# Kernel tuning notes

Measured on AMD Instinct MI355X. Metric: run time of the kernel, lower is better.

## Reference

```python
import jax, jax.numpy as jnp
import numpy as np

# FP4 (E2M1) code table: nibble = [sign(1) | exp(2) | mantissa(1)]
# magnitudes for codes 0..7: 0, 0.5, 1, 1.5, 2, 3, 4, 6; codes 8..15 are negated.
_MAG = np.array([0.0, 0.5, 1.0, 1.5, 2.0, 3.0, 4.0, 6.0], dtype=np.float32)
FP4_LUT = jnp.asarray(np.concatenate([_MAG, -_MAG]))  # [16]

BLOCK = 16  # scale-factor block size along in_features


def setup_inputs() -> dict:
    key = jax.random.key(0)
    k0, k1, k2, k3, k4 = jax.random.split(key, 5)
    M, K, N = 32, 8192, 8192  # tokens, in_features, out_features
    inp = jax.random.normal(k0, (M, K), dtype=jnp.float32)
    qweight = jax.random.randint(k1, (N, K // 2), 0, 256, dtype=jnp.int32)  # packed FP4 pairs
    scales = jax.random.uniform(k2, (N, K // BLOCK), dtype=jnp.float32)      # per-block scales
    amax = jax.random.uniform(k3, (1,), dtype=jnp.float32) + 0.5             # global scale
    bias = jax.random.normal(k4, (N,), dtype=jnp.float32)
    return {"input": inp, "qweight": qweight, "scales": scales, "amax": amax, "bias": bias}


def _dequantize(qweight, scales, amax):
    N = qweight.shape[0]
    low = qweight & 0xF            # first element of each pair
    high = (qweight >> 4) & 0xF    # second element
    nibbles = jnp.stack([low, high], axis=-1).reshape(N, -1)  # [N, K]
    vals = FP4_LUT[nibbles]                                   # [N, K] fp4 values
    # per-block scaling: block of BLOCK contiguous in-features shares one scale
    w = (vals.reshape(N, -1, BLOCK) * scales[..., None]).reshape(N, -1)
    return w * amax[0]


def reference(input, qweight, scales, amax, bias):
    weight = _dequantize(qweight, scales, amax)   # [N, K] full-precision weight
    return input @ weight.T + bias                # F.linear
```

## Files before the change

### kernel.cpp

```cpp
#include <hip/hip_runtime.h>
#include <hip/hip_bf16.h>

#define M_DIM 32
#define K_DIM 8192
#define N_DIM 8192
#define KS 16
#define KCH (K_DIM / KS)
#define STEPS (KCH / 32)
#define NPB 128
#define NBLK (N_DIM / NPB)
#define MAIN_BLOCKS (NBLK * KS)

#define QW_ROWI4 (K_DIM / 8)
#define SC_ROW (K_DIM / 16)

#define QROW 65
#define AROW 520
#define SROW 34

typedef _Float16 half8   __attribute__((ext_vector_type(8)));
typedef _Float16 half4_t __attribute__((ext_vector_type(4)));
typedef float    floatx4 __attribute__((ext_vector_type(4)));

__device__ __forceinline__ uint32_t dec2(uint32_t b) {
  uint32_t c0 = b & 0xFu, c1 = (b >> 4) & 0xFu;
  uint32_t m0 = c0 & 7u, m1 = c1 & 7u;
  uint32_t t0 = min(28u * m0, m0 + 28u);
  uint32_t t1 = min(28u * m1, m1 + 28u);
  return (t0 << 9) | ((c0 & 8u) << 12)
       | (t1 << 25) | ((c1 & 8u) << 28);
}

__device__ __forceinline__ half8 decode8p(uint32_t q, _Float16 s) {
  union { uint32_t u[4]; half8 h; } w;
  w.u[0] = dec2(q & 0xFFu);
  w.u[1] = dec2((q >> 8) & 0xFFu);
  w.u[2] = dec2((q >> 16) & 0xFFu);
  w.u[3] = dec2((q >> 24) & 0xFFu);
  half8 sv = {s, s, s, s, s, s, s, s};
  return w.h * sv;
}

__global__ void init_out_kernel(floatx4* __restrict__ out4,
                                const floatx4* __restrict__ bias4) {
  int idx = blockIdx.x * blockDim.x + threadIdx.x;
  out4[idx] = bias4[idx & (N_DIM / 4 - 1)];
}

__global__ void reduce_kernel(const floatx4* __restrict__ part,
                              const floatx4* __restrict__ bias4,
                              floatx4* __restrict__ out4) {
  int idx = blockIdx.x * blockDim.x + threadIdx.x;
  floatx4 acc = bias4[idx & (N_DIM / 4 - 1)];
#pragma unroll
  for (int s = 0; s < KS; ++s)
    acc += part[(size_t)s * (M_DIM * N_DIM / 4) + idx];
  out4[idx] = acc;
}

template <bool PARTIAL>
__global__ __launch_bounds__(256, 2) void fp4_linear_kernel(
    const float* __restrict__ inp,
    const int4*  __restrict__ qw4,
    const float* __restrict__ scales,
    const float* __restrict__ amaxp,
    float* __restrict__ outp)
{
  __shared__ uint32_t Qs[NPB * QROW];
  __shared__ _Float16 As[M_DIM * AROW];
  __shared__ _Float16 Ss[NPB * SROW];

  const int t    = threadIdx.x;
  const int lane = t & 63;
  const int w    = t >> 6;
  const int ks   = blockIdx.x & (KS - 1);
  const int nb   = blockIdx.x >> 4;
  const int n0   = nb * NPB;
  const float amax = amaxp[0];

  {
    const int4* qbase = qw4 + (size_t)ks * (KCH / 8);
    for (int g = 0; g < 4; ++g) {
      int4 tmp[8];
#pragma unroll
      for (int j = 0; j < 8; ++j) {
        const int r = w * 32 + g * 8 + j;
        tmp[j] = qbase[(size_t)(n0 + r) * QW_ROWI4 + lane];
      }
#pragma unroll
      for (int j = 0; j < 8; ++j) {
        const int r = w * 32 + g * 8 + j;
        uint32_t pk = ((uint32_t)tmp[j].x & 0xFFu)
                    | (((uint32_t)tmp[j].y & 0xFFu) << 8)
                    | (((uint32_t)tmp[j].z & 0xFFu) << 16)
                    | (((uint32_t)tmp[j].w & 0xFFu) << 24);
        Qs[r * QROW + lane] = pk;
      }
    }
  }

  {
    for (int g = 0; g < 2; ++g) {
      floatx4 tmp[8];
#pragma unroll
      for (int j = 0; j < 4; ++j) {
        const int r = w * 8 + g * 4 + j;
        const floatx4* ab =
            reinterpret_cast<const floatx4*>(inp + (size_t)r * K_DIM + ks * KCH);
        tmp[2 * j]     = ab[lane];
        tmp[2 * j + 1] = ab[lane + 64];
      }
#pragma unroll
      for (int j = 0; j < 4; ++j) {
        const int r = w * 8 + g * 4 + j;
        floatx4 f0 = tmp[2 * j], f1 = tmp[2 * j + 1];
        half4_t h0, h1;
        h0[0] = (_Float16)f0[0]; h0[1] = (_Float16)f0[1];
        h0[2] = (_Float16)f0[2]; h0[3] = (_Float16)f0[3];
        h1[0] = (_Float16)f1[0]; h1[1] = (_Float16)f1[1];
        h1[2] = (_Float16)f1[2]; h1[3] = (_Float16)f1[3];
        *(half4_t*)&As[r * AROW + lane * 4]        = h0;
        *(half4_t*)&As[r * AROW + (lane + 64) * 4] = h1;
      }
    }
  }

  {
#pragma unroll
    for (int j = 0; j < 4; ++j) {
      const int idx = j * 256 + t;
      const int r = idx >> 3, c = idx & 7;
      floatx4 f = reinterpret_cast<const floatx4*>(
          scales + (size_t)(n0 + r) * SC_ROW + ks * (KCH / 16))[c];
      half4_t h;
      h[0] = (_Float16)(f[0] * amax); h[1] = (_Float16)(f[1] * amax);
      h[2] = (_Float16)(f[2] * amax); h[3] = (_Float16)(f[3] * amax);
      *(half4_t*)&Ss[r * SROW + c * 4] = h;
    }
  }
  __syncthreads();

  const int row  = lane & 15;
  const int quad = lane >> 4;
  const int nloc = w * 32;

  const uint32_t* qAp = &Qs[(nloc + row) * QROW];
  const uint32_t* qBp = &Qs[(nloc + 16 + row) * QROW];
  const _Float16* a0p = &As[row * AROW];
  const _Float16* a1p = &As[(row + 16) * AROW];
  const _Float16* sAp = &Ss[(nloc + row) * SROW];
  const _Float16* sBp = &Ss[(nloc + 16 + row) * SROW];

  floatx4 acc00 = {0.f, 0.f, 0.f, 0.f};
  floatx4 acc01 = {0.f, 0.f, 0.f, 0.f};
  floatx4 acc10 = {0.f, 0.f, 0.f, 0.f};
  floatx4 acc11 = {0.f, 0.f, 0.f, 0.f};

#pragma unroll
  for (int it = 0; it < STEPS; ++it) {
    const uint32_t qA = qAp[it * 4 + quad];
    const uint32_t qB = qBp[it * 4 + quad];
    const _Float16 sA = sAp[it * 2 + (quad >> 1)];
    const _Float16 sB = sBp[it * 2 + (quad >> 1)];
    half8 bA = decode8p(qA, sA);
    half8 bB = decode8p(qB, sB);
    half8 a0 = *(const half8*)(a0p + it * 32 + quad * 8);
    half8 a1 = *(const half8*)(a1p + it * 32 + quad * 8);
    acc00 = __builtin_amdgcn_mfma_f32_16x16x32_f16(a0, bA, acc00, 0, 0, 0);
    acc01 = __builtin_amdgcn_mfma_f32_16x16x32_f16(a0, bB, acc01, 0, 0, 0);
    acc10 = __builtin_amdgcn_mfma_f32_16x16x32_f16(a1, bA, acc10, 0, 0, 0);
    acc11 = __builtin_amdgcn_mfma_f32_16x16x32_f16(a1, bB, acc11, 0, 0, 0);
  }

  if (PARTIAL) {
    float* pb = outp + (size_t)ks * (M_DIM * N_DIM);
#pragma unroll
    for (int r = 0; r < 4; ++r) {
      const int m = quad * 4 + r;
      float* o0 = pb + (size_t)m * N_DIM + n0 + nloc;
      float* o1 = pb + (size_t)(m + 16) * N_DIM + n0 + nloc;
      o0[row]      = acc00[r];
      o0[16 + row] = acc01[r];
      o1[row]      = acc10[r];
      o1[16 + row] = acc11[r];
    }
  } else {
#pragma unroll
    for (int r = 0; r < 4; ++r) {
      const int m = quad * 4 + r;
      float* o0 = outp + (size_t)m * N_DIM + n0 + nloc;
      float* o1 = outp + (size_t)(m + 16) * N_DIM + n0 + nloc;
      unsafeAtomicAdd(o0 + row,      acc00[r]);
      unsafeAtomicAdd(o0 + 16 + row, acc01[r]);
      unsafeAtomicAdd(o1 + row,      acc10[r]);
      unsafeAtomicAdd(o1 + 16 + row, acc11[r]);
    }
  }
}

extern "C" void kernel_launch(void* const* d_in, const int* in_sizes, int n_in,
                              void* d_out, int out_size, void* d_ws, size_t ws_size,
                              hipStream_t stream) {
  const float* inp    = (const float*)d_in[0];
  const int4*  qw4    = (const int4*)d_in[1];
  const float* scales = (const float*)d_in[2];
  const float* amaxp  = (const float*)d_in[3];
  const float* bias   = (const float*)d_in[4];
  float* out = (float*)d_out;

  const size_t part_bytes = (size_t)KS * M_DIM * N_DIM * sizeof(float);
  if (ws_size >= part_bytes) {
    float* part = (float*)d_ws;
    fp4_linear_kernel<true><<<MAIN_BLOCKS, 256, 0, stream>>>(
        inp, qw4, scales, amaxp, part);
    reduce_kernel<<<M_DIM * N_DIM / 4 / 256, 256, 0, stream>>>(
        (const floatx4*)part, (const floatx4*)bias, (floatx4*)out);
  } else {
    init_out_kernel<<<M_DIM * N_DIM / 4 / 256, 256, 0, stream>>>(
        (floatx4*)out, (const floatx4*)bias);
    fp4_linear_kernel<false><<<MAIN_BLOCKS, 256, 0, stream>>>(
        inp, qw4, scales, amaxp, out);
  }
}
```

Before: 224.4 us.

## Restructure split-K decomposition with fp16 activation pre-pass and in-block wave reduction

Changes the split-K layout from 16 K-slices with 128 output columns per block to 2 K-halves with 16 columns per block. Each wave now handles a quarter of the block's K range and the four waves are reduced through shared memory. A separate kernel converts the activations to fp16 once, and the main kernel then reads them straight from global memory instead of staging them per block. XOR swizzling is added to the weight and scale shared arrays. This shrinks the partial-sum buffer and the final reduction and raises occupancy. The costs are an extra launch, reliance on the workspace being large enough with the fallback path removed, and reading A from global memory without shared-memory reuse.

```diff
diff --git a/kernel.cpp b/kernel.cpp
--- a/kernel.cpp
+++ b/kernel.cpp
@@ -4,22 +4,16 @@
 #define M_DIM 32
 #define K_DIM 8192
 #define N_DIM 8192
-#define KS 16
-#define KCH (K_DIM / KS)
-#define STEPS (KCH / 32)
-#define NPB 128
-#define NBLK (N_DIM / NPB)
-#define MAIN_BLOCKS (NBLK * KS)
+#define KS 2
+#define KHALF (K_DIM / KS)
+#define NRPB 16
+#define MAIN_BLOCKS ((N_DIM / NRPB) * KS)
 
 #define QW_ROWI4 (K_DIM / 8)
 #define SC_ROW (K_DIM / 16)
 
-#define QROW 65
-#define AROW 520
-#define SROW 34
-
 typedef _Float16 half8   __attribute__((ext_vector_type(8)));
-typedef _Float16 half4_t __attribute__((ext_vector_type(4)));
+typedef _Float16 half2_t __attribute__((ext_vector_type(2)));
 typedef float    floatx4 __attribute__((ext_vector_type(4)));
 
 __device__ __forceinline__ uint32_t dec2(uint32_t b) {
@@ -41,86 +35,63 @@
   return w.h * sv;
 }
 
-__global__ void init_out_kernel(floatx4* __restrict__ out4,
-                                const floatx4* __restrict__ bias4) {
+typedef _Float16 half4_t __attribute__((ext_vector_type(4)));
+
+__global__ void convertA_kernel(const floatx4* __restrict__ in4,
+                                half4_t* __restrict__ out4) {
   int idx = blockIdx.x * blockDim.x + threadIdx.x;
-  out4[idx] = bias4[idx & (N_DIM / 4 - 1)];
+  floatx4 f = in4[idx];
+  half4_t h;
+  h[0] = (_Float16)f[0]; h[1] = (_Float16)f[1];
+  h[2] = (_Float16)f[2]; h[3] = (_Float16)f[3];
+  out4[idx] = h;
 }
 
 __global__ void reduce_kernel(const floatx4* __restrict__ part,
                               const floatx4* __restrict__ bias4,
                               floatx4* __restrict__ out4) {
   int idx = blockIdx.x * blockDim.x + threadIdx.x;
-  floatx4 acc = bias4[idx & (N_DIM / 4 - 1)];
-#pragma unroll
-  for (int s = 0; s < KS; ++s)
-    acc += part[(size_t)s * (M_DIM * N_DIM / 4) + idx];
-  out4[idx] = acc;
+  out4[idx] = bias4[idx & (N_DIM / 4 - 1)]
+            + part[idx] + part[(M_DIM * N_DIM / 4) + idx];
 }
 
-template <bool PARTIAL>
-__global__ __launch_bounds__(256, 2) void fp4_linear_kernel(
-    const float* __restrict__ inp,
-    const int4*  __restrict__ qw4,
-    const float* __restrict__ scales,
-    const float* __restrict__ amaxp,
-    float* __restrict__ outp)
+__global__ __launch_bounds__(256, 4) void fp4_linear_kernel(
+    const int4*     __restrict__ qw4,
+    const float*    __restrict__ scales,
+    const float*    __restrict__ amaxp,
+    const _Float16* __restrict__ Af16,
+    float*          __restrict__ part)
 {
-  __shared__ uint32_t Qs[NPB * QROW];
-  __shared__ _Float16 As[M_DIM * AROW];
-  __shared__ _Float16 Ss[NPB * SROW];
+  __shared__ uint32_t Qs[NRPB * 512];
+  __shared__ _Float16 Ss[NRPB * 256];
 
   const int t    = threadIdx.x;
   const int lane = t & 63;
   const int w    = t >> 6;
-  const int ks   = blockIdx.x & (KS - 1);
-  const int nb   = blockIdx.x >> 4;
-  const int n0   = nb * NPB;
+  const int ks   = blockIdx.x & 1;
+  const int g    = blockIdx.x >> 1;
+  const int n0   = g * NRPB;
   const float amax = amaxp[0];
 
   {
-    const int4* qbase = qw4 + (size_t)ks * (KCH / 8);
-    for (int g = 0; g < 4; ++g) {
+    const int4* src = qw4 + (size_t)ks * (KHALF / 8);
+    for (int gq = 0; gq < 4; ++gq) {
       int4 tmp[8];
 #pragma unroll
       for (int j = 0; j < 8; ++j) {
-        const int r = w * 32 + g * 8 + j;
-        tmp[j] = qbase[(size_t)(n0 + r) * QW_ROWI4 + lane];
+        const int flat = (gq * 8 + j) * 256 + t;
+        const int r = flat >> 9, col = flat & 511;
+        tmp[j] = src[(size_t)(n0 + r) * QW_ROWI4 + col];
       }
 #pragma unroll
       for (int j = 0; j < 8; ++j) {
-        const int r = w * 32 + g * 8 + j;
+        const int flat = (gq * 8 + j) * 256 + t;
+        const int r = flat >> 9, col = flat & 511;
         uint32_t pk = ((uint32_t)tmp[j].x & 0xFFu)
                     | (((uint32_t)tmp[j].y & 0xFFu) << 8)
                     | (((uint32_t)tmp[j].z & 0xFFu) << 16)
                     | (((uint32_t)tmp[j].w & 0xFFu) << 24);
-        Qs[r * QROW + lane] = pk;
-      }
-    }
-  }
-
-  {
-    for (int g = 0; g < 2; ++g) {
-      floatx4 tmp[8];
-#pragma unroll
-      for (int j = 0; j < 4; ++j) {
-        const int r = w * 8 + g * 4 + j;
-        const floatx4* ab =
-            reinterpret_cast<const floatx4*>(inp + (size_t)r * K_DIM + ks * KCH);
-        tmp[2 * j]     = ab[lane];
-        tmp[2 * j + 1] = ab[lane + 64];
-      }
-#pragma unroll
-      for (int j = 0; j < 4; ++j) {
-        const int r = w * 8 + g * 4 + j;
-        floatx4 f0 = tmp[2 * j], f1 = tmp[2 * j + 1];
-        half4_t h0, h1;
-        h0[0] = (_Float16)f0[0]; h0[1] = (_Float16)f0[1];
-        h0[2] = (_Float16)f0[2]; h0[3] = (_Float16)f0[3];
-        h1[0] = (_Float16)f1[0]; h1[1] = (_Float16)f1[1];
-        h1[2] = (_Float16)f1[2]; h1[3] = (_Float16)f1[3];
-        *(half4_t*)&As[r * AROW + lane * 4]        = h0;
-        *(half4_t*)&As[r * AROW + (lane + 64) * 4] = h1;
+        Qs[r * 512 + (col ^ r)] = pk;
       }
     }
   }
@@ -128,73 +99,62 @@
   {
 #pragma unroll
     for (int j = 0; j < 4; ++j) {
-      const int idx = j * 256 + t;
-      const int r = idx >> 3, c = idx & 7;
+      const int flat = j * 256 + t;
+      const int r = flat >> 6, c4 = flat & 63;
       floatx4 f = reinterpret_cast<const floatx4*>(
-          scales + (size_t)(n0 + r) * SC_ROW + ks * (KCH / 16))[c];
-      half4_t h;
-      h[0] = (_Float16)(f[0] * amax); h[1] = (_Float16)(f[1] * amax);
-      h[2] = (_Float16)(f[2] * amax); h[3] = (_Float16)(f[3] * amax);
-      *(half4_t*)&Ss[r * SROW + c * 4] = h;
+          scales + (size_t)(n0 + r) * SC_ROW + ks * (KHALF / 16))[c4];
+#pragma unroll
+      for (int i = 0; i < 2; ++i) {
+        const int p = c4 * 2 + i;
+        half2_t h2 = {(_Float16)(f[2 * i] * amax),
+                      (_Float16)(f[2 * i + 1] * amax)};
+        *(half2_t*)&Ss[r * 256 + (p ^ r) * 2] = h2;
+      }
     }
   }
   __syncthreads();
 
   const int row  = lane & 15;
   const int quad = lane >> 4;
-  const int nloc = w * 32;
+  const uint32_t* qrow = &Qs[row * 512];
+  const _Float16* srow = &Ss[row * 256];
+  const _Float16* a0p = Af16 + (size_t)row * K_DIM + ks * KHALF + w * 1024;
+  const _Float16* a1p = a0p + (size_t)16 * K_DIM;
 
-  const uint32_t* qAp = &Qs[(nloc + row) * QROW];
-  const uint32_t* qBp = &Qs[(nloc + 16 + row) * QROW];
-  const _Float16* a0p = &As[row * AROW];
-  const _Float16* a1p = &As[(row + 16) * AROW];
-  const _Float16* sAp = &Ss[(nloc + row) * SROW];
-  const _Float16* sBp = &Ss[(nloc + 16 + row) * SROW];
+  floatx4 acc0 = {0.f, 0.f, 0.f, 0.f};
+  floatx4 acc1 = {0.f, 0.f, 0.f, 0.f};
 
-  floatx4 acc00 = {0.f, 0.f, 0.f, 0.f};
-  floatx4 acc01 = {0.f, 0.f, 0.f, 0.f};
-  floatx4 acc10 = {0.f, 0.f, 0.f, 0.f};
-  floatx4 acc11 = {0.f, 0.f, 0.f, 0.f};
-
-#pragma unroll
-  for (int it = 0; it < STEPS; ++it) {
-    const uint32_t qA = qAp[it * 4 + quad];
-    const uint32_t qB = qBp[it * 4 + quad];
-    const _Float16 sA = sAp[it * 2 + (quad >> 1)];
-    const _Float16 sB = sBp[it * 2 + (quad >> 1)];
-    half8 bA = decode8p(qA, sA);
-    half8 bB = decode8p(qB, sB);
+#pragma unroll 4
+  for (int it = 0; it < 32; ++it) {
+    const uint32_t q = qrow[(w * 128 + it * 4 + quad) ^ row];
+    const _Float16 s = srow[(((w * 32 + it) ^ row) * 2) + (quad >> 1)];
+    half8 b  = decode8p(q, s);
     half8 a0 = *(const half8*)(a0p + it * 32 + quad * 8);
     half8 a1 = *(const half8*)(a1p + it * 32 + quad * 8);
-    acc00 = __builtin_amdgcn_mfma_f32_16x16x32_f16(a0, bA, acc00, 0, 0, 0);
-    acc01 = __builtin_amdgcn_mfma_f32_16x16x32_f16(a0, bB, acc01, 0, 0, 0);
-    acc10 = __builtin_amdgcn_mfma_f32_16x16x32_f16(a1, bA, acc10, 0, 0, 0);
-    acc11 = __builtin_amdgcn_mfma_f32_16x16x32_f16(a1, bB, acc11, 0, 0, 0);
+    acc0 = __builtin_amdgcn_mfma_f32_16x16x32_f16(a0, b, acc0, 0, 0, 0);
+    acc1 = __builtin_amdgcn_mfma_f32_16x16x32_f16(a1, b, acc1, 0, 0, 0);
   }
 
-  if (PARTIAL) {
-    float* pb = outp + (size_t)ks * (M_DIM * N_DIM);
+  __syncthreads();
+  float* red = (float*)Qs;
+  {
+    float* slab = red + w * (32 * 18);
 #pragma unroll
-    for (int r = 0; r < 4; ++r) {
-      const int m = quad * 4 + r;
-      float* o0 = pb + (size_t)m * N_DIM + n0 + nloc;
-      float* o1 = pb + (size_t)(m + 16) * N_DIM + n0 + nloc;
-      o0[row]      = acc00[r];
-      o0[16 + row] = acc01[r];
-      o1[row]      = acc10[r];
-      o1[16 + row] = acc11[r];
+    for (int r4 = 0; r4 < 4; ++r4) {
+      const int m = quad * 4 + r4;
+      slab[m * 18 + row]        = acc0[r4];
+      slab[(m + 16) * 18 + row] = acc1[r4];
     }
-  } else {
+  }
+  __syncthreads();
+  float* pb = part + (size_t)ks * (M_DIM * N_DIM);
 #pragma unroll
-    for (int r = 0; r < 4; ++r) {
-      const int m = quad * 4 + r;
-      float* o0 = outp + (size_t)m * N_DIM + n0 + nloc;
-      float* o1 = outp + (size_t)(m + 16) * N_DIM + n0 + nloc;
-      unsafeAtomicAdd(o0 + row,      acc00[r]);
-      unsafeAtomicAdd(o0 + 16 + row, acc01[r]);
-      unsafeAtomicAdd(o1 + row,      acc10[r]);
-      unsafeAtomicAdd(o1 + 16 + row, acc11[r]);
-    }
+  for (int i = 0; i < 2; ++i) {
+    const int o = i * 256 + t;
+    const int m = o >> 4, n = o & 15;
+    float v = red[m * 18 + n] + red[576 + m * 18 + n]
+            + red[2 * 576 + m * 18 + n] + red[3 * 576 + m * 18 + n];
+    pb[(size_t)m * N_DIM + n0 + n] = v;
   }
 }
 
@@ -208,17 +168,13 @@
   const float* bias   = (const float*)d_in[4];
   float* out = (float*)d_out;
 
-  const size_t part_bytes = (size_t)KS * M_DIM * N_DIM * sizeof(float);
-  if (ws_size >= part_bytes) {
-    float* part = (float*)d_ws;
-    fp4_linear_kernel<true><<<MAIN_BLOCKS, 256, 0, stream>>>(
-        inp, qw4, scales, amaxp, part);
-    reduce_kernel<<<M_DIM * N_DIM / 4 / 256, 256, 0, stream>>>(
-        (const floatx4*)part, (const floatx4*)bias, (floatx4*)out);
-  } else {
-    init_out_kernel<<<M_DIM * N_DIM / 4 / 256, 256, 0, stream>>>(
-        (floatx4*)out, (const floatx4*)bias);
-    fp4_linear_kernel<false><<<MAIN_BLOCKS, 256, 0, stream>>>(
-        inp, qw4, scales, amaxp, out);
-  }
+  _Float16* Af16 = (_Float16*)d_ws;
+  float*    part = (float*)((char*)d_ws + (size_t)M_DIM * K_DIM * sizeof(_Float16));
+
+  convertA_kernel<<<M_DIM * K_DIM / 4 / 256, 256, 0, stream>>>(
+      (const floatx4*)inp, (half4_t*)Af16);
+  fp4_linear_kernel<<<MAIN_BLOCKS, 256, 0, stream>>>(
+      qw4, scales, amaxp, Af16, part);
+  reduce_kernel<<<M_DIM * N_DIM / 4 / 256, 256, 0, stream>>>(
+      (const floatx4*)part, (const floatx4*)bias, (floatx4*)out);
 }
```

Result: slower. 239.0 us (+6.5%).

## Software-pipeline K chunks through registers and pre-convert activations to fp16

Applied to the files above, without the earlier changes.

The main kernel now walks its K slice in 128-wide chunks instead of staging the whole slice in LDS at once. Each chunk's global loads are prefetched into registers while the MFMA loop runs on the previous chunk, and LDS drops from about 60KB to a few KB so launch bounds can rise to 4 blocks per SM. A separate kernel converts the activations to fp16 once, so the main kernel stops reconverting them per block. The atomic fallback path is removed: the kernel always writes partials to the workspace and runs the reduce, which assumes the workspace is large enough.

```diff
diff --git a/kernel.cpp b/kernel.cpp
--- a/kernel.cpp
+++ b/kernel.cpp
@@ -6,17 +6,18 @@
 #define N_DIM 8192
 #define KS 16
 #define KCH (K_DIM / KS)
-#define STEPS (KCH / 32)
+#define CHK 128
+#define NCHK (KCH / CHK)
+#define STEPS (CHK / 32)
 #define NPB 128
-#define NBLK (N_DIM / NPB)
-#define MAIN_BLOCKS (NBLK * KS)
+#define MAIN_BLOCKS ((N_DIM / NPB) * KS)
 
 #define QW_ROWI4 (K_DIM / 8)
 #define SC_ROW (K_DIM / 16)
 
-#define QROW 65
-#define AROW 520
-#define SROW 34
+#define QROW 17
+#define AROW 136
+#define SROW 9
 
 typedef _Float16 half8   __attribute__((ext_vector_type(8)));
 typedef _Float16 half4_t __attribute__((ext_vector_type(4)));
@@ -41,10 +42,14 @@
   return w.h * sv;
 }
 
-__global__ void init_out_kernel(floatx4* __restrict__ out4,
-                                const floatx4* __restrict__ bias4) {
+__global__ void convertA_kernel(const floatx4* __restrict__ in4,
+                                half4_t* __restrict__ out4) {
   int idx = blockIdx.x * blockDim.x + threadIdx.x;
-  out4[idx] = bias4[idx & (N_DIM / 4 - 1)];
+  floatx4 f = in4[idx];
+  half4_t h;
+  h[0] = (_Float16)f[0]; h[1] = (_Float16)f[1];
+  h[2] = (_Float16)f[2]; h[3] = (_Float16)f[3];
+  out4[idx] = h;
 }
 
 __global__ void reduce_kernel(const floatx4* __restrict__ part,
@@ -58,17 +63,17 @@
   out4[idx] = acc;
 }
 
-template <bool PARTIAL>
-__global__ __launch_bounds__(256, 2) void fp4_linear_kernel(
-    const float* __restrict__ inp,
+template <bool F16A>
+__global__ __launch_bounds__(256, 4) void fp4_linear_kernel(
+    const void*  __restrict__ Av,
     const int4*  __restrict__ qw4,
     const float* __restrict__ scales,
     const float* __restrict__ amaxp,
-    float* __restrict__ outp)
+    float*       __restrict__ part)
 {
   __shared__ uint32_t Qs[NPB * QROW];
   __shared__ _Float16 As[M_DIM * AROW];
-  __shared__ _Float16 Ss[NPB * SROW];
+  __shared__ float    Ss[NPB * SROW];
 
   const int t    = threadIdx.x;
   const int lane = t & 63;
@@ -76,125 +81,131 @@
   const int ks   = blockIdx.x & (KS - 1);
   const int nb   = blockIdx.x >> 4;
   const int n0   = nb * NPB;
+  const int kb   = ks * KCH;
   const float amax = amaxp[0];
 
+  const int qr = t >> 4, qc = t & 15;
+  const int4* qsrc = qw4 + (size_t)(n0 + qr) * QW_ROWI4 + ks * (KCH / 8) + qc;
+  const int sr = t >> 1, sh = t & 1;
+  const float* ssrc = scales + (size_t)(n0 + sr) * SC_ROW + ks * (KCH / 16) + sh * 4;
+  const int ar16 = t >> 4, ac16 = t & 15;
+  const _Float16* asrc16 =
+      (const _Float16*)Av + (size_t)ar16 * K_DIM + kb + ac16 * 8;
+  const int ar32 = t >> 5, ac32 = t & 31;
+  const float* asrc32 = (const float*)Av + (size_t)ar32 * K_DIM + kb + ac32 * 4;
+
+  int4    qreg[8];
+  half8   areg16[2];
+  floatx4 areg32[4];
+  floatx4 sreg;
+
   {
-    const int4* qbase = qw4 + (size_t)ks * (KCH / 8);
-    for (int g = 0; g < 4; ++g) {
-      int4 tmp[8];
-#pragma unroll
-      for (int j = 0; j < 8; ++j) {
-        const int r = w * 32 + g * 8 + j;
-        tmp[j] = qbase[(size_t)(n0 + r) * QW_ROWI4 + lane];
-      }
-#pragma unroll
-      for (int j = 0; j < 8; ++j) {
-        const int r = w * 32 + g * 8 + j;
-        uint32_t pk = ((uint32_t)tmp[j].x & 0xFFu)
-                    | (((uint32_t)tmp[j].y & 0xFFu) << 8)
-                    | (((uint32_t)tmp[j].z & 0xFFu) << 16)
-                    | (((uint32_t)tmp[j].w & 0xFFu) << 24);
-        Qs[r * QROW + lane] = pk;
-      }
-    }
-  }
-
-  {
-    for (int g = 0; g < 2; ++g) {
-      floatx4 tmp[8];
-#pragma unroll
-      for (int j = 0; j < 4; ++j) {
-        const int r = w * 8 + g * 4 + j;
-        const floatx4* ab =
-            reinterpret_cast<const floatx4*>(inp + (size_t)r * K_DIM + ks * KCH);
-        tmp[2 * j]     = ab[lane];
-        tmp[2 * j + 1] = ab[lane + 64];
-      }
-#pragma unroll
-      for (int j = 0; j < 4; ++j) {
-        const int r = w * 8 + g * 4 + j;
-        floatx4 f0 = tmp[2 * j], f1 = tmp[2 * j + 1];
-        half4_t h0, h1;
-        h0[0] = (_Float16)f0[0]; h0[1] = (_Float16)f0[1];
-        h0[2] = (_Float16)f0[2]; h0[3] = (_Float16)f0[3];
-        h1[0] = (_Float16)f1[0]; h1[1] = (_Float16)f1[1];
-        h1[2] = (_Float16)f1[2]; h1[3] = (_Float16)f1[3];
-        *(half4_t*)&As[r * AROW + lane * 4]        = h0;
-        *(half4_t*)&As[r * AROW + (lane + 64) * 4] = h1;
-      }
-    }
-  }
-
-  {
-#pragma unroll
-    for (int j = 0; j < 4; ++j) {
-      const int idx = j * 256 + t;
-      const int r = idx >> 3, c = idx & 7;
-      floatx4 f = reinterpret_cast<const floatx4*>(
-          scales + (size_t)(n0 + r) * SC_ROW + ks * (KCH / 16))[c];
-      half4_t h;
-      h[0] = (_Float16)(f[0] * amax); h[1] = (_Float16)(f[1] * amax);
-      h[2] = (_Float16)(f[2] * amax); h[3] = (_Float16)(f[3] * amax);
-      *(half4_t*)&Ss[r * SROW + c * 4] = h;
-    }
-  }
-  __syncthreads();
+#pragma unroll
+    for (int j = 0; j < 8; ++j)
+      qreg[j] = qsrc[(size_t)j * 16 * QW_ROWI4];
+    if (F16A) {
+#pragma unroll
+      for (int j = 0; j < 2; ++j)
+        areg16[j] = *(const half8*)(asrc16 + (size_t)j * 16 * K_DIM);
+    } else {
+#pragma unroll
+      for (int j = 0; j < 4; ++j)
+        areg32[j] = *(const floatx4*)(asrc32 + (size_t)j * 8 * K_DIM);
+    }
+    sreg = *(const floatx4*)ssrc;
+  }
 
   const int row  = lane & 15;
   const int quad = lane >> 4;
   const int nloc = w * 32;
-
   const uint32_t* qAp = &Qs[(nloc + row) * QROW];
   const uint32_t* qBp = &Qs[(nloc + 16 + row) * QROW];
   const _Float16* a0p = &As[row * AROW];
   const _Float16* a1p = &As[(row + 16) * AROW];
-  const _Float16* sAp = &Ss[(nloc + row) * SROW];
-  const _Float16* sBp = &Ss[(nloc + 16 + row) * SROW];
+  const float*    sAp = &Ss[(nloc + row) * SROW];
+  const float*    sBp = &Ss[(nloc + 16 + row) * SROW];
 
   floatx4 acc00 = {0.f, 0.f, 0.f, 0.f};
   floatx4 acc01 = {0.f, 0.f, 0.f, 0.f};
   floatx4 acc10 = {0.f, 0.f, 0.f, 0.f};
   floatx4 acc11 = {0.f, 0.f, 0.f, 0.f};
 
-#pragma unroll
-  for (int it = 0; it < STEPS; ++it) {
-    const uint32_t qA = qAp[it * 4 + quad];
-    const uint32_t qB = qBp[it * 4 + quad];
-    const _Float16 sA = sAp[it * 2 + (quad >> 1)];
-    const _Float16 sB = sBp[it * 2 + (quad >> 1)];
-    half8 bA = decode8p(qA, sA);
-    half8 bB = decode8p(qB, sB);
-    half8 a0 = *(const half8*)(a0p + it * 32 + quad * 8);
-    half8 a1 = *(const half8*)(a1p + it * 32 + quad * 8);
-    acc00 = __builtin_amdgcn_mfma_f32_16x16x32_f16(a0, bA, acc00, 0, 0, 0);
-    acc01 = __builtin_amdgcn_mfma_f32_16x16x32_f16(a0, bB, acc01, 0, 0, 0);
-    acc10 = __builtin_amdgcn_mfma_f32_16x16x32_f16(a1, bA, acc10, 0, 0, 0);
-    acc11 = __builtin_amdgcn_mfma_f32_16x16x32_f16(a1, bB, acc11, 0, 0, 0);
-  }
-
-  if (PARTIAL) {
-    float* pb = outp + (size_t)ks * (M_DIM * N_DIM);
-#pragma unroll
-    for (int r = 0; r < 4; ++r) {
-      const int m = quad * 4 + r;
-      float* o0 = pb + (size_t)m * N_DIM + n0 + nloc;
-      float* o1 = pb + (size_t)(m + 16) * N_DIM + n0 + nloc;
-      o0[row]      = acc00[r];
-      o0[16 + row] = acc01[r];
-      o1[row]      = acc10[r];
-      o1[16 + row] = acc11[r];
-    }
-  } else {
-#pragma unroll
-    for (int r = 0; r < 4; ++r) {
-      const int m = quad * 4 + r;
-      float* o0 = outp + (size_t)m * N_DIM + n0 + nloc;
-      float* o1 = outp + (size_t)(m + 16) * N_DIM + n0 + nloc;
-      unsafeAtomicAdd(o0 + row,      acc00[r]);
-      unsafeAtomicAdd(o0 + 16 + row, acc01[r]);
-      unsafeAtomicAdd(o1 + row,      acc10[r]);
-      unsafeAtomicAdd(o1 + 16 + row, acc11[r]);
-    }
+  for (int c = 0; c < NCHK; ++c) {
+    if (c) __syncthreads();
+
+#pragma unroll
+    for (int j = 0; j < 8; ++j) {
+      uint32_t pk = ((uint32_t)qreg[j].x & 0xFFu)
+                  | (((uint32_t)qreg[j].y & 0xFFu) << 8)
+                  | (((uint32_t)qreg[j].z & 0xFFu) << 16)
+                  | (((uint32_t)qreg[j].w & 0xFFu) << 24);
+      Qs[(j * 16 + qr) * QROW + qc] = pk;
+    }
+    if (F16A) {
+#pragma unroll
+      for (int j = 0; j < 2; ++j)
+        *(half8*)&As[(j * 16 + ar16) * AROW + ac16 * 8] = areg16[j];
+    } else {
+#pragma unroll
+      for (int j = 0; j < 4; ++j) {
+        floatx4 f = areg32[j];
+        half4_t h;
+        h[0] = (_Float16)f[0]; h[1] = (_Float16)f[1];
+        h[2] = (_Float16)f[2]; h[3] = (_Float16)f[3];
+        *(half4_t*)&As[(j * 8 + ar32) * AROW + ac32 * 4] = h;
+      }
+    }
+    {
+      float* sd = &Ss[sr * SROW + sh * 4];
+      sd[0] = sreg[0] * amax; sd[1] = sreg[1] * amax;
+      sd[2] = sreg[2] * amax; sd[3] = sreg[3] * amax;
+    }
+    __syncthreads();
+
+    if (c + 1 < NCHK) {
+      const int co = c + 1;
+#pragma unroll
+      for (int j = 0; j < 8; ++j)
+        qreg[j] = qsrc[(size_t)j * 16 * QW_ROWI4 + co * (CHK / 8)];
+      if (F16A) {
+#pragma unroll
+        for (int j = 0; j < 2; ++j)
+          areg16[j] = *(const half8*)(asrc16 + (size_t)j * 16 * K_DIM + co * CHK);
+      } else {
+#pragma unroll
+        for (int j = 0; j < 4; ++j)
+          areg32[j] = *(const floatx4*)(asrc32 + (size_t)j * 8 * K_DIM + co * CHK);
+      }
+      sreg = *(const floatx4*)(ssrc + co * (CHK / 16));
+    }
+
+#pragma unroll
+    for (int it = 0; it < STEPS; ++it) {
+      const uint32_t qA = qAp[it * 4 + quad];
+      const uint32_t qB = qBp[it * 4 + quad];
+      const _Float16 sA = (_Float16)sAp[it * 2 + (quad >> 1)];
+      const _Float16 sB = (_Float16)sBp[it * 2 + (quad >> 1)];
+      half8 bA = decode8p(qA, sA);
+      half8 bB = decode8p(qB, sB);
+      half8 a0 = *(const half8*)(a0p + it * 32 + quad * 8);
+      half8 a1 = *(const half8*)(a1p + it * 32 + quad * 8);
+      acc00 = __builtin_amdgcn_mfma_f32_16x16x32_f16(a0, bA, acc00, 0, 0, 0);
+      acc01 = __builtin_amdgcn_mfma_f32_16x16x32_f16(a0, bB, acc01, 0, 0, 0);
+      acc10 = __builtin_amdgcn_mfma_f32_16x16x32_f16(a1, bA, acc10, 0, 0, 0);
+      acc11 = __builtin_amdgcn_mfma_f32_16x16x32_f16(a1, bB, acc11, 0, 0, 0);
+    }
+  }
+
+  float* pb = part + (size_t)ks * (M_DIM * N_DIM);
+#pragma unroll
+  for (int r = 0; r < 4; ++r) {
+    const int m = quad * 4 + r;
+    float* o0 = pb + (size_t)m * N_DIM + n0 + nloc;
+    float* o1 = pb + (size_t)(m + 16) * N_DIM + n0 + nloc;
+    o0[row]      = acc00[r];
+    o0[16 + row] = acc01[r];
+    o1[row]      = acc10[r];
+    o1[16 + row] = acc11[r];
   }
 }
 
@@ -209,16 +220,19 @@
   float* out = (float*)d_out;
 
   const size_t part_bytes = (size_t)KS * M_DIM * N_DIM * sizeof(float);
-  if (ws_size >= part_bytes) {
-    float* part = (float*)d_ws;
+  const size_t a16_bytes  = (size_t)M_DIM * K_DIM * sizeof(_Float16);
+  float* partp = (float*)d_ws;
+
+  if (ws_size >= part_bytes + a16_bytes) {
+    _Float16* Af16 = (_Float16*)((char*)d_ws + part_bytes);
+    convertA_kernel<<<M_DIM * K_DIM / 4 / 256, 256, 0, stream>>>(
+        (const floatx4*)inp, (half4_t*)Af16);
     fp4_linear_kernel<true><<<MAIN_BLOCKS, 256, 0, stream>>>(
-        inp, qw4, scales, amaxp, part);
-    reduce_kernel<<<M_DIM * N_DIM / 4 / 256, 256, 0, stream>>>(
-        (const floatx4*)part, (const floatx4*)bias, (floatx4*)out);
+        Af16, qw4, scales, amaxp, partp);
   } else {
-    init_out_kernel<<<M_DIM * N_DIM / 4 / 256, 256, 0, stream>>>(
-        (floatx4*)out, (const floatx4*)bias);
     fp4_linear_kernel<false><<<MAIN_BLOCKS, 256, 0, stream>>>(
-        inp, qw4, scales, amaxp, out);
-  }
-}
+        inp, qw4, scales, amaxp, partp);
+  }
+  reduce_kernel<<<M_DIM * N_DIM / 4 / 256, 256, 0, stream>>>(
+      (const floatx4*)partp, (const floatx4*)bias, (floatx4*)out);
+}
```

New measurement: 219.3 us. 2.3% less time.
